# Kernel tuning notes

Measured on AMD Instinct MI355X. Metric: run time of the kernel, lower is better.

The kernel has to match this reference:

```python
import jax, jax.numpy as jnp
import numpy as np

BT = 64  # chunk size (BLOCK_SIZE_C)
EPS = 1e-06


def setup_inputs() -> dict:
    key = jax.random.key(0)
    k1, k2, k3, k4 = jax.random.split(key, 4)
    B, H, S, D = 4, 8, 4096, 128
    q = jax.random.normal(k1, (B, H, S, D), dtype=jnp.float32)
    k = jax.random.normal(k2, (B, H, S, D), dtype=jnp.float32)
    v = jax.random.normal(k3, (B, H, S, D), dtype=jnp.float32)
    beta = jax.random.uniform(k4, (B, H, S), dtype=jnp.float32)
    return {"q": q, "k": k, "v": v, "beta": beta}


def _chunk_gated_delta_fwd(q, k, v, beta):
    # Recurrence: S_t = beta_t * S_{t-1} + k_t (x) v_t ;  o_t = q_t @ S_t
    B, H, S, D = q.shape
    NC = S // BT
    f32 = jnp.float32
    qf = q.astype(f32).reshape(B, H, NC, BT, D)
    kf = k.astype(f32).reshape(B, H, NC, BT, D)
    vf = v.astype(f32).reshape(B, H, NC, BT, D)
    log_beta = jnp.log(beta.astype(f32).reshape(B, H, NC, BT) + EPS)
    cum = jnp.cumsum(log_beta, axis=-1)                     # [B,H,NC,BT]
    tot = cum[..., -1]                                      # [B,H,NC]
    decay_from_start = jnp.exp(cum)                         # [B,H,NC,BT]
    decay_to_end = jnp.exp(tot[..., None] - cum)            # [B,H,NC,BT]
    causal = jnp.tril(jnp.ones((BT, BT), dtype=bool))
    decay_matrix = jnp.exp(cum[..., :, None] - cum[..., None, :])  # [B,H,NC,BT,BT]
    decay_masked = jnp.where(causal, decay_matrix, 0.0)
    # intra-chunk contribution (fully parallel across chunks)
    qk = jnp.einsum('bhcid,bhcjd->bhcij', qf, kf)
    out_intra = jnp.einsum('bhcij,bhcjd->bhcid', qk * decay_masked, vf)
    # per-chunk state-update term: (k * decay_to_end)^T @ v
    upd = jnp.einsum('bhcid,bhcie->bhcde', kf * decay_to_end[..., None], vf)
    # sequential inter-chunk recurrence over chunks
    def step(state, xs):
        qc, dfs_c, tot_c, upd_c = xs
        out_inter = jnp.einsum('bhid,bhde->bhie', qc * dfs_c[..., None], state)
        new_state = state * jnp.exp(tot_c)[..., None, None] + upd_c
        return new_state, out_inter
    xs = (jnp.moveaxis(qf, 2, 0), jnp.moveaxis(decay_from_start, 2, 0),
          jnp.moveaxis(tot, 2, 0), jnp.moveaxis(upd, 2, 0))
    state0 = jnp.zeros((B, H, D, D), dtype=f32)
    _, out_inter = jax.lax.scan(step, state0, xs)           # [NC,B,H,BT,D]
    out = out_intra + jnp.moveaxis(out_inter, 0, 2)
    return out.reshape(B, H, S, D).astype(q.dtype)


def reference(q, k, v, beta):
    return _chunk_gated_delta_fwd(q, k, v, beta)
```

## Files before the change

### kernel.cpp

```cpp
#include <hip/hip_runtime.h>
#include <hip/hip_bf16.h>
#include <math.h>

#define Gp  32
#define Sp  4096
#define Dp  128
#define BTp 64
#define NCp 64

typedef __attribute__((ext_vector_type(8))) short bf16x8;
typedef __attribute__((ext_vector_type(4))) float f32x4;

#define MFMA(a,b,c) __builtin_amdgcn_mfma_f32_16x16x32_bf16((a),(b),(c),0,0,0)

#define TSWZ(d, slot) ((((slot) ^ (((d) & 15) >> 1)) << 3))

__device__ inline unsigned pack2(float lo, float hi) {
    __hip_bfloat162 h = __float22bfloat162_rn(make_float2(lo, hi));
    union { __hip_bfloat162 v; unsigned u; } t; t.v = h; return t.u;
}
__device__ inline float bflo(unsigned u) { union { unsigned u; float f; } t; t.u = u << 16; return t.f; }
__device__ inline float bfhi(unsigned u) { union { unsigned u; float f; } t; t.u = u & 0xffff0000u; return t.f; }

__global__ __launch_bounds__(256) void gdn_beta(
    const float* __restrict__ beta, float* __restrict__ cum_buf,
    float* __restrict__ dte_buf, float* __restrict__ dfs_buf,
    float* __restrict__ tot_buf)
{
    const int tid = threadIdx.x, lane = tid & 63, w = tid >> 6;
    const int cc = blockIdx.x * 4 + w;
    const int g = cc >> 6, c = cc & 63;
    const size_t bbase = (size_t)g * Sp + (size_t)c * BTp;
    float x = logf(beta[bbase + lane] + 1e-6f);
    #pragma unroll
    for (int off = 1; off < 64; off <<= 1) {
        float n = __shfl_up(x, off, 64);
        if (lane >= off) x += n;
    }
    const float tot = __shfl(x, 63, 64);
    cum_buf[bbase + lane] = x;
    dfs_buf[bbase + lane] = expf(x);
    dte_buf[bbase + lane] = expf(tot - x);
    if (lane == 63) tot_buf[g * NCp + c] = tot;
}

__global__ __launch_bounds__(256, 3) void gdn_intra(
    const float* __restrict__ q, const float* __restrict__ k,
    const float* __restrict__ v, const float* __restrict__ cum_buf,
    const float* __restrict__ dte_buf,
    float* __restrict__ out, unsigned short* __restrict__ outi,
    unsigned short* __restrict__ upd)
{
    __shared__ unsigned short s_k [64 * 128];
    __shared__ unsigned short s_vt[128 * 64];
    __shared__ unsigned short s_kt[128 * 64];

    const int blk = blockIdx.x, g = blk >> 6, c = blk & 63;
    const int tid = threadIdx.x, lane = tid & 63, w = tid >> 6;
    const int m16 = lane & 15, quad = lane >> 4;
    const size_t base  = ((size_t)g * Sp + (size_t)c * BTp) * Dp;
    const size_t bbase = (size_t)g * Sp + (size_t)c * BTp;

    const float x = cum_buf[bbase + lane];

    const int dd = 4 * (tid & 31);
    const int rg = tid >> 5;
    const int i0 = 8 * rg;
    const float* kp = k + base + (size_t)i0 * Dp + dd;
    const float* vp = v + base + (size_t)i0 * Dp + dd;
    float4 kx[8], vx[8];
    #pragma unroll
    for (int r = 0; r < 8; ++r) kx[r] = *(const float4*)(kp + (size_t)r * Dp);
    #pragma unroll
    for (int r = 0; r < 8; ++r) vx[r] = *(const float4*)(vp + (size_t)r * Dp);
    const float4 dt0 = *(const float4*)(dte_buf + bbase + i0);
    const float4 dt1 = *(const float4*)(dte_buf + bbase + i0 + 4);

    const float* qrow = q + base + (size_t)(16 * w + m16) * Dp + quad * 8;
    float4 qa[4], qb[4];
    #pragma unroll
    for (int ks = 0; ks < 4; ++ks) {
        qa[ks] = *(const float4*)(qrow + ks * 32);
        qb[ks] = *(const float4*)(qrow + ks * 32 + 4);
    }

    #pragma unroll
    for (int r = 0; r < 8; ++r) {
        const int i = i0 + r;
        const int ad = i * 128 + (((dd >> 3) ^ (i & 15)) << 3) + (dd & 7);
        uint2 pw; pw.x = pack2(kx[r].x, kx[r].y); pw.y = pack2(kx[r].z, kx[r].w);
        *(uint2*)&s_k[ad] = pw;
    }

    {
        uint4 t;
        t.x = pack2(vx[0].x, vx[1].x); t.y = pack2(vx[2].x, vx[3].x);
        t.z = pack2(vx[4].x, vx[5].x); t.w = pack2(vx[6].x, vx[7].x);
        *(uint4*)&s_vt[(dd + 0) * 64 + TSWZ(dd + 0, rg)] = t;
        t.x = pack2(vx[0].y, vx[1].y); t.y = pack2(vx[2].y, vx[3].y);
        t.z = pack2(vx[4].y, vx[5].y); t.w = pack2(vx[6].y, vx[7].y);
        *(uint4*)&s_vt[(dd + 1) * 64 + TSWZ(dd + 1, rg)] = t;
        t.x = pack2(vx[0].z, vx[1].z); t.y = pack2(vx[2].z, vx[3].z);
        t.z = pack2(vx[4].z, vx[5].z); t.w = pack2(vx[6].z, vx[7].z);
        *(uint4*)&s_vt[(dd + 2) * 64 + TSWZ(dd + 2, rg)] = t;
        t.x = pack2(vx[0].w, vx[1].w); t.y = pack2(vx[2].w, vx[3].w);
        t.z = pack2(vx[4].w, vx[5].w); t.w = pack2(vx[6].w, vx[7].w);
        *(uint4*)&s_vt[(dd + 3) * 64 + TSWZ(dd + 3, rg)] = t;
    }

    {
        const float d0 = dt0.x, d1 = dt0.y, d2 = dt0.z, d3 = dt0.w;
        const float d4 = dt1.x, d5 = dt1.y, d6 = dt1.z, d7 = dt1.w;
        uint4 t;
        t.x = pack2(kx[0].x * d0, kx[1].x * d1); t.y = pack2(kx[2].x * d2, kx[3].x * d3);
        t.z = pack2(kx[4].x * d4, kx[5].x * d5); t.w = pack2(kx[6].x * d6, kx[7].x * d7);
        *(uint4*)&s_kt[(dd + 0) * 64 + TSWZ(dd + 0, rg)] = t;
        t.x = pack2(kx[0].y * d0, kx[1].y * d1); t.y = pack2(kx[2].y * d2, kx[3].y * d3);
        t.z = pack2(kx[4].y * d4, kx[5].y * d5); t.w = pack2(kx[6].y * d6, kx[7].y * d7);
        *(uint4*)&s_kt[(dd + 1) * 64 + TSWZ(dd + 1, rg)] = t;
        t.x = pack2(kx[0].z * d0, kx[1].z * d1); t.y = pack2(kx[2].z * d2, kx[3].z * d3);
        t.z = pack2(kx[4].z * d4, kx[5].z * d5); t.w = pack2(kx[6].z * d6, kx[7].z * d7);
        *(uint4*)&s_kt[(dd + 2) * 64 + TSWZ(dd + 2, rg)] = t;
        t.x = pack2(kx[0].w * d0, kx[1].w * d1); t.y = pack2(kx[2].w * d2, kx[3].w * d3);
        t.z = pack2(kx[4].w * d4, kx[5].w * d5); t.w = pack2(kx[6].w * d6, kx[7].w * d7);
        *(uint4*)&s_kt[(dd + 3) * 64 + TSWZ(dd + 3, rg)] = t;
    }

    bf16x8 qf[4];
    #pragma unroll
    for (int ks = 0; ks < 4; ++ks) {
        union { bf16x8 v; unsigned ui[4]; } t;
        t.ui[0] = pack2(qa[ks].x, qa[ks].y); t.ui[1] = pack2(qa[ks].z, qa[ks].w);
        t.ui[2] = pack2(qb[ks].x, qb[ks].y); t.ui[3] = pack2(qb[ks].z, qb[ks].w);
        qf[ks] = t.v;
    }

    __syncthreads();

    f32x4 accP[4] = {};
    #pragma unroll
    for (int nt = 0; nt < 4; ++nt) {
        if (nt <= w) {
            #pragma unroll
            for (int ks = 0; ks < 4; ++ks) {
                const bf16x8 kf = *(const bf16x8*)&s_k[(16 * nt + m16) * 128 + (((quad + 4 * ks) ^ m16) << 3)];
                accP[nt] = MFMA(kf, qf[ks], accP[nt]);
            }
        }
    }

    const float ci = __shfl(x, 16 * w + m16, 64);
    unsigned p_pk[4][2];
    #pragma unroll
    for (int nt = 0; nt < 4; ++nt) { p_pk[nt][0] = 0u; p_pk[nt][1] = 0u; }
    #pragma unroll
    for (int nt = 0; nt < 4; ++nt) {
        if (nt <= w) {
            float pm[4];
            #pragma unroll
            for (int r = 0; r < 4; ++r) {
                const int j = 16 * nt + 4 * quad + r;
                const float cj = __shfl(x, j, 64);
                float val = accP[nt][r] * expf(ci - cj);
                if (nt == w) val = (16 * w + m16 >= j) ? val : 0.f;
                pm[r] = val;
            }
            p_pk[nt][0] = pack2(pm[0], pm[1]);
            p_pk[nt][1] = pack2(pm[2], pm[3]);
        }
    }

    bf16x8 af[2];
    #pragma unroll
    for (int ks = 0; ks < 2; ++ks) {
        if (ks <= (w >> 1)) {
            union { bf16x8 v; unsigned ui[4]; } t;
            #pragma unroll
            for (int m = 0; m < 4; ++m) {
                const int src = m16 + 16 * (2 * (quad & 1) + (m >> 1));
                const unsigned aA = (unsigned)__shfl((int)p_pk[2 * ks][m & 1], src, 64);
                const unsigned aB = (unsigned)__shfl((int)p_pk[2 * ks + 1][m & 1], src, 64);
                t.ui[m] = (quad >> 1) ? aB : aA;
            }
            af[ks] = t.v;
        }
    }

    {
        f32x4 accU[2][8] = {};
        #pragma unroll
        for (int ks = 0; ks < 2; ++ks) {
            const int sw = TSWZ(m16, quad + 4 * ks);
            const bf16x8 b0 = *(const bf16x8*)&s_vt[(16 * (2 * w)     + m16) * 64 + sw];
            const bf16x8 b1 = *(const bf16x8*)&s_vt[(16 * (2 * w + 1) + m16) * 64 + sw];
            #pragma unroll
            for (int nt = 0; nt < 8; ++nt) {
                const bf16x8 a = *(const bf16x8*)&s_kt[(16 * nt + m16) * 64 + sw];
                accU[0][nt] = MFMA(a, b0, accU[0][nt]);
                accU[1][nt] = MFMA(a, b1, accU[1][nt]);
            }
        }
        unsigned short* ub = upd + (size_t)blk * Dp * Dp;
        #pragma unroll
        for (int mt = 0; mt < 2; ++mt) {
            const int e = 16 * (2 * w + mt) + m16;
            #pragma unroll
            for (int nt = 0; nt < 8; ++nt) {
                uint2 pw;
                pw.x = pack2(accU[mt][nt][0], accU[mt][nt][1]);
                pw.y = pack2(accU[mt][nt][2], accU[mt][nt][3]);
                *(uint2*)&ub[(size_t)e * Dp + 16 * nt + 4 * quad] = pw;
            }
        }
    }

    {
        f32x4 accO[8] = {};
        #pragma unroll
        for (int ks = 0; ks < 2; ++ks) {
            if (ks <= (w >> 1)) {
                const int sw = TSWZ(m16, quad + 4 * ks);
                #pragma unroll
                for (int nt = 0; nt < 8; ++nt) {
                    const bf16x8 a = *(const bf16x8*)&s_vt[(16 * nt + m16) * 64 + sw];
                    accO[nt] = MFMA(a, af[ks], accO[nt]);
                }
            }
        }
        const int i = 16 * w + m16;
        if (outi) {
            #pragma unroll
            for (int nt = 0; nt < 8; ++nt) {
                uint2 pw;
                pw.x = pack2(accO[nt][0], accO[nt][1]);
                pw.y = pack2(accO[nt][2], accO[nt][3]);
                *(uint2*)&outi[base + (size_t)i * Dp + 16 * nt + 4 * quad] = pw;
            }
        } else {
            #pragma unroll
            for (int nt = 0; nt < 8; ++nt) {
                float4 st;
                st.x = accO[nt][0]; st.y = accO[nt][1];
                st.z = accO[nt][2]; st.w = accO[nt][3];
                *(float4*)&out[base + (size_t)i * Dp + 16 * nt + 4 * quad] = st;
            }
        }
    }
}

__global__ __launch_bounds__(128) void gdn_scan(
    unsigned short* __restrict__ upd, const float* __restrict__ tot_buf)
{
    const int g = blockIdx.x >> 4, slab = blockIdx.x & 15, tid = threadIdx.x;
    __shared__ float s_e[NCp];
    if (tid < NCp) s_e[tid] = expf(tot_buf[g * NCp + tid]);
    __syncthreads();
    uint4* b = (uint4*)(upd + (size_t)g * NCp * Dp * Dp) + slab * 128 + tid;
    float s0 = 0.f, s1 = 0.f, s2 = 0.f, s3 = 0.f;
    float s4 = 0.f, s5 = 0.f, s6 = 0.f, s7 = 0.f;
    uint4 pf[4];
    #pragma unroll
    for (int j = 0; j < 4; ++j) pf[j] = b[(size_t)j * 2048];
    #pragma unroll
    for (int cc = 0; cc < NCp; ++cc) {
        const uint4 cur = pf[cc & 3];
        if (cc + 4 < NCp) pf[cc & 3] = b[(size_t)(cc + 4) * 2048];
        const float e = s_e[cc];
        uint4 stq;
        stq.x = pack2(s0, s1); stq.y = pack2(s2, s3);
        stq.z = pack2(s4, s5); stq.w = pack2(s6, s7);
        b[(size_t)cc * 2048] = stq;
        s0 = s0 * e + bflo(cur.x); s1 = s1 * e + bfhi(cur.x);
        s2 = s2 * e + bflo(cur.y); s3 = s3 * e + bfhi(cur.y);
        s4 = s4 * e + bflo(cur.z); s5 = s5 * e + bfhi(cur.z);
        s6 = s6 * e + bflo(cur.w); s7 = s7 * e + bfhi(cur.w);
    }
}

__global__ __launch_bounds__(256) void gdn_inter(
    const float* __restrict__ q, const unsigned short* __restrict__ state,
    const float* __restrict__ dfs_buf, const unsigned short* __restrict__ outi,
    float* __restrict__ out)
{
    const int blk = blockIdx.x, g = blk >> 6, c = blk & 63;
    const int tid = threadIdx.x, lane = tid & 63, w = tid >> 6;
    const int m16 = lane & 15, quad = lane >> 4;
    const size_t base  = ((size_t)g * Sp + (size_t)c * BTp) * Dp;
    const size_t bbase = (size_t)g * Sp + (size_t)c * BTp;
    const unsigned short* sb = state + (size_t)blk * Dp * Dp;
    const int i = 16 * w + m16;

    const float scale = dfs_buf[bbase + i];
    bf16x8 qf[4];
    const float* qrow = q + base + (size_t)i * Dp + quad * 8;
    #pragma unroll
    for (int ks = 0; ks < 4; ++ks) {
        const float4 a = *(const float4*)(qrow + ks * 32);
        const float4 b = *(const float4*)(qrow + ks * 32 + 4);
        union { bf16x8 v; unsigned ui[4]; } t;
        t.ui[0] = pack2(a.x * scale, a.y * scale);
        t.ui[1] = pack2(a.z * scale, a.w * scale);
        t.ui[2] = pack2(b.x * scale, b.y * scale);
        t.ui[3] = pack2(b.z * scale, b.w * scale);
        qf[ks] = t.v;
    }

    float ovf[8][4];
    if (outi) {
        #pragma unroll
        for (int nt = 0; nt < 8; ++nt) {
            const uint2 pw = *(const uint2*)&outi[base + (size_t)i * Dp + 16 * nt + 4 * quad];
            ovf[nt][0] = bflo(pw.x); ovf[nt][1] = bfhi(pw.x);
            ovf[nt][2] = bflo(pw.y); ovf[nt][3] = bfhi(pw.y);
        }
    } else {
        #pragma unroll
        for (int nt = 0; nt < 8; ++nt) {
            const float4 o = *(const float4*)&out[base + (size_t)i * Dp + 16 * nt + 4 * quad];
            ovf[nt][0] = o.x; ovf[nt][1] = o.y; ovf[nt][2] = o.z; ovf[nt][3] = o.w;
        }
    }

    f32x4 acc[8] = {};
    #pragma unroll
    for (int ks = 0; ks < 4; ++ks) {
        bf16x8 afr[8];
        #pragma unroll
        for (int nt = 0; nt < 8; ++nt)
            afr[nt] = *(const bf16x8*)(sb + (16 * nt + m16) * Dp + quad * 8 + ks * 32);
        #pragma unroll
        for (int nt = 0; nt < 8; ++nt)
            acc[nt] = MFMA(afr[nt], qf[ks], acc[nt]);
    }
    #pragma unroll
    for (int nt = 0; nt < 8; ++nt) {
        float4 st;
        st.x = ovf[nt][0] + acc[nt][0]; st.y = ovf[nt][1] + acc[nt][1];
        st.z = ovf[nt][2] + acc[nt][2]; st.w = ovf[nt][3] + acc[nt][3];
        *(float4*)&out[base + (size_t)i * Dp + 16 * nt + 4 * quad] = st;
    }
}

extern "C" void kernel_launch(void* const* d_in, const int* in_sizes, int n_in,
                              void* d_out, int out_size, void* d_ws, size_t ws_size,
                              hipStream_t stream) {
    const float* q    = (const float*)d_in[0];
    const float* k    = (const float*)d_in[1];
    const float* v    = (const float*)d_in[2];
    const float* beta = (const float*)d_in[3];
    float* out = (float*)d_out;

    unsigned short* upd = (unsigned short*)d_ws;
    float* tot_buf = (float*)(upd + (size_t)Gp * NCp * Dp * Dp);
    float* dfs_buf = tot_buf + Gp * NCp;
    float* cum_buf = dfs_buf + (size_t)Gp * Sp;
    float* dte_buf = cum_buf + (size_t)Gp * Sp;
    unsigned short* outi = (unsigned short*)(dte_buf + (size_t)Gp * Sp);
    const size_t need = (size_t)((char*)(outi + (size_t)Gp * Sp * Dp) - (char*)d_ws);
    if (ws_size < need) outi = nullptr;

    gdn_beta <<<Gp * NCp / 4, 256, 0, stream>>>(beta, cum_buf, dte_buf, dfs_buf, tot_buf);
    gdn_intra<<<Gp * NCp, 256, 0, stream>>>(q, k, v, cum_buf, dte_buf, out, outi, upd);
    gdn_scan <<<Gp * 16, 128, 0, stream>>>(upd, tot_buf);
    gdn_inter<<<Gp * NCp, 256, 0, stream>>>(q, upd, dfs_buf, outi, out);
}
```

Baseline: 302.1 us.

## Process two chunks per intra block with prefetch and cache scaled bf16 q

The intra kernel now handles two consecutive chunks per block. It loads the second chunk's k/v/q into registers while the first chunk is being computed, so global-load latency can overlap with MFMA work. The intra kernel also writes a decay-scaled bf16 copy of q to the workspace, so the inter kernel reads half the bytes and skips the rescale. The costs are more register pressure (launch bounds drop from 3 to 2 blocks per CU), half as many blocks, extra workspace writes, and rounding q to bf16 twice.

Result: slower. 310.0 us (+2.6%).

```diff
diff --git a/kernel.cpp b/kernel.cpp
--- a/kernel.cpp
+++ b/kernel.cpp
@@ -44,46 +44,13 @@
     if (lane == 63) tot_buf[g * NCp + c] = tot;
 }
 
-__global__ __launch_bounds__(256, 3) void gdn_intra(
-    const float* __restrict__ q, const float* __restrict__ k,
-    const float* __restrict__ v, const float* __restrict__ cum_buf,
-    const float* __restrict__ dte_buf,
-    float* __restrict__ out, unsigned short* __restrict__ outi,
-    unsigned short* __restrict__ upd)
-{
-    __shared__ unsigned short s_k [64 * 128];
-    __shared__ unsigned short s_vt[128 * 64];
-    __shared__ unsigned short s_kt[128 * 64];
-
-    const int blk = blockIdx.x, g = blk >> 6, c = blk & 63;
-    const int tid = threadIdx.x, lane = tid & 63, w = tid >> 6;
-    const int m16 = lane & 15, quad = lane >> 4;
-    const size_t base  = ((size_t)g * Sp + (size_t)c * BTp) * Dp;
-    const size_t bbase = (size_t)g * Sp + (size_t)c * BTp;
-
-    const float x = cum_buf[bbase + lane];
-
-    const int dd = 4 * (tid & 31);
-    const int rg = tid >> 5;
+__device__ __forceinline__ void stage_chunk(
+    unsigned short* __restrict__ s_k, unsigned short* __restrict__ s_vt,
+    unsigned short* __restrict__ s_kt,
+    int dd, int rg, const float4* kx, const float4* vx,
+    const float4 dt0, const float4 dt1)
+{
     const int i0 = 8 * rg;
-    const float* kp = k + base + (size_t)i0 * Dp + dd;
-    const float* vp = v + base + (size_t)i0 * Dp + dd;
-    float4 kx[8], vx[8];
-    #pragma unroll
-    for (int r = 0; r < 8; ++r) kx[r] = *(const float4*)(kp + (size_t)r * Dp);
-    #pragma unroll
-    for (int r = 0; r < 8; ++r) vx[r] = *(const float4*)(vp + (size_t)r * Dp);
-    const float4 dt0 = *(const float4*)(dte_buf + bbase + i0);
-    const float4 dt1 = *(const float4*)(dte_buf + bbase + i0 + 4);
-
-    const float* qrow = q + base + (size_t)(16 * w + m16) * Dp + quad * 8;
-    float4 qa[4], qb[4];
-    #pragma unroll
-    for (int ks = 0; ks < 4; ++ks) {
-        qa[ks] = *(const float4*)(qrow + ks * 32);
-        qb[ks] = *(const float4*)(qrow + ks * 32 + 4);
-    }
-
     #pragma unroll
     for (int r = 0; r < 8; ++r) {
         const int i = i0 + r;
@@ -91,7 +58,6 @@
         uint2 pw; pw.x = pack2(kx[r].x, kx[r].y); pw.y = pack2(kx[r].z, kx[r].w);
         *(uint2*)&s_k[ad] = pw;
     }
-
     {
         uint4 t;
         t.x = pack2(vx[0].x, vx[1].x); t.y = pack2(vx[2].x, vx[3].x);
@@ -107,7 +73,6 @@
         t.z = pack2(vx[4].w, vx[5].w); t.w = pack2(vx[6].w, vx[7].w);
         *(uint4*)&s_vt[(dd + 3) * 64 + TSWZ(dd + 3, rg)] = t;
     }
-
     {
         const float d0 = dt0.x, d1 = dt0.y, d2 = dt0.z, d3 = dt0.w;
         const float d4 = dt1.x, d5 = dt1.y, d6 = dt1.z, d7 = dt1.w;
@@ -125,8 +90,10 @@
         t.z = pack2(kx[4].w * d4, kx[5].w * d5); t.w = pack2(kx[6].w * d6, kx[7].w * d7);
         *(uint4*)&s_kt[(dd + 3) * 64 + TSWZ(dd + 3, rg)] = t;
     }
-
-    bf16x8 qf[4];
+}
+
+__device__ __forceinline__ void pack_q(const float4* qa, const float4* qb, bf16x8* qf)
+{
     #pragma unroll
     for (int ks = 0; ks < 4; ++ks) {
         union { bf16x8 v; unsigned ui[4]; } t;
@@ -134,9 +101,17 @@
         t.ui[2] = pack2(qb[ks].x, qb[ks].y); t.ui[3] = pack2(qb[ks].z, qb[ks].w);
         qf[ks] = t.v;
     }
-
-    __syncthreads();
-
+}
+
+__device__ __forceinline__ void intra_compute(
+    const float x, const bf16x8* qf,
+    const unsigned short* s_k, const unsigned short* s_vt,
+    const unsigned short* s_kt,
+    const int w, const int m16, const int quad,
+    const size_t base, const size_t cid,
+    float* __restrict__ out, unsigned short* __restrict__ outi,
+    unsigned short* __restrict__ upd, unsigned short* __restrict__ qs)
+{
     f32x4 accP[4] = {};
     #pragma unroll
     for (int nt = 0; nt < 4; ++nt) {
@@ -170,6 +145,20 @@
         }
     }
 
+    if (qs) {
+        const float sc = expf(ci);
+        #pragma unroll
+        for (int ks = 0; ks < 4; ++ks) {
+            union { bf16x8 v; unsigned ui[4]; } t; t.v = qf[ks];
+            uint4 o;
+            o.x = pack2(bflo(t.ui[0]) * sc, bfhi(t.ui[0]) * sc);
+            o.y = pack2(bflo(t.ui[1]) * sc, bfhi(t.ui[1]) * sc);
+            o.z = pack2(bflo(t.ui[2]) * sc, bfhi(t.ui[2]) * sc);
+            o.w = pack2(bflo(t.ui[3]) * sc, bfhi(t.ui[3]) * sc);
+            *(uint4*)&qs[base + (size_t)(16 * w + m16) * Dp + quad * 8 + ks * 32] = o;
+        }
+    }
+
     bf16x8 af[2];
     #pragma unroll
     for (int ks = 0; ks < 2; ++ks) {
@@ -200,7 +189,7 @@
                 accU[1][nt] = MFMA(a, b1, accU[1][nt]);
             }
         }
-        unsigned short* ub = upd + (size_t)blk * Dp * Dp;
+        unsigned short* ub = upd + cid * (size_t)(Dp * Dp);
         #pragma unroll
         for (int mt = 0; mt < 2; ++mt) {
             const int e = 16 * (2 * w + mt) + m16;
@@ -246,6 +235,93 @@
             }
         }
     }
+}
+
+__global__ __launch_bounds__(256, 2) void gdn_intra(
+    const float* __restrict__ q, const float* __restrict__ k,
+    const float* __restrict__ v, const float* __restrict__ cum_buf,
+    const float* __restrict__ dte_buf,
+    float* __restrict__ out, unsigned short* __restrict__ outi,
+    unsigned short* __restrict__ upd, unsigned short* __restrict__ qs)
+{
+    __shared__ unsigned short s_k [64 * 128];
+    __shared__ unsigned short s_vt[128 * 64];
+    __shared__ unsigned short s_kt[128 * 64];
+
+    const int blk = blockIdx.x, g = blk >> 5, pr = blk & 31;
+    const int c0 = 2 * pr;
+    const int tid = threadIdx.x, lane = tid & 63, w = tid >> 6;
+    const int m16 = lane & 15, quad = lane >> 4;
+    const int dd = 4 * (tid & 31), rg = tid >> 5, i0 = 8 * rg;
+
+    const size_t cid0  = (size_t)g * NCp + c0, cid1 = cid0 + 1;
+    const size_t bb0   = (size_t)g * Sp + (size_t)c0 * BTp, bb1 = bb0 + BTp;
+    const size_t base0 = bb0 * Dp, base1 = bb1 * Dp;
+
+    const float x0 = cum_buf[bb0 + lane];
+    float4 kx[8], vx[8];
+    {
+        const float* kp = k + base0 + (size_t)i0 * Dp + dd;
+        const float* vp = v + base0 + (size_t)i0 * Dp + dd;
+        #pragma unroll
+        for (int r = 0; r < 8; ++r) kx[r] = *(const float4*)(kp + (size_t)r * Dp);
+        #pragma unroll
+        for (int r = 0; r < 8; ++r) vx[r] = *(const float4*)(vp + (size_t)r * Dp);
+    }
+    const float4 dt00 = *(const float4*)(dte_buf + bb0 + i0);
+    const float4 dt01 = *(const float4*)(dte_buf + bb0 + i0 + 4);
+    float4 qa[4], qb[4];
+    {
+        const float* qrow = q + base0 + (size_t)(16 * w + m16) * Dp + quad * 8;
+        #pragma unroll
+        for (int ks = 0; ks < 4; ++ks) {
+            qa[ks] = *(const float4*)(qrow + ks * 32);
+            qb[ks] = *(const float4*)(qrow + ks * 32 + 4);
+        }
+    }
+
+    stage_chunk(s_k, s_vt, s_kt, dd, rg, kx, vx, dt00, dt01);
+    bf16x8 qf0[4];
+    pack_q(qa, qb, qf0);
+
+    const float x1 = cum_buf[bb1 + lane];
+    float4 kx1[8], vx1[8];
+    {
+        const float* kp = k + base1 + (size_t)i0 * Dp + dd;
+        const float* vp = v + base1 + (size_t)i0 * Dp + dd;
+        #pragma unroll
+        for (int r = 0; r < 8; ++r) kx1[r] = *(const float4*)(kp + (size_t)r * Dp);
+        #pragma unroll
+        for (int r = 0; r < 8; ++r) vx1[r] = *(const float4*)(vp + (size_t)r * Dp);
+    }
+    const float4 dt10 = *(const float4*)(dte_buf + bb1 + i0);
+    const float4 dt11 = *(const float4*)(dte_buf + bb1 + i0 + 4);
+
+    __syncthreads();
+
+    float4 qa1[4], qb1[4];
+    {
+        const float* qrow = q + base1 + (size_t)(16 * w + m16) * Dp + quad * 8;
+        #pragma unroll
+        for (int ks = 0; ks < 4; ++ks) {
+            qa1[ks] = *(const float4*)(qrow + ks * 32);
+            qb1[ks] = *(const float4*)(qrow + ks * 32 + 4);
+        }
+    }
+
+    intra_compute(x0, qf0, s_k, s_vt, s_kt, w, m16, quad,
+                  base0, cid0, out, outi, upd, qs);
+
+    __syncthreads();
+
+    stage_chunk(s_k, s_vt, s_kt, dd, rg, kx1, vx1, dt10, dt11);
+    bf16x8 qf1[4];
+    pack_q(qa1, qb1, qf1);
+
+    __syncthreads();
+
+    intra_compute(x1, qf1, s_k, s_vt, s_kt, w, m16, quad,
+                  base1, cid1, out, outi, upd, qs);
 }
 
 __global__ __launch_bounds__(128) void gdn_scan(
@@ -280,7 +356,7 @@
 __global__ __launch_bounds__(256) void gdn_inter(
     const float* __restrict__ q, const unsigned short* __restrict__ state,
     const float* __restrict__ dfs_buf, const unsigned short* __restrict__ outi,
-    float* __restrict__ out)
+    const unsigned short* __restrict__ qs, float* __restrict__ out)
 {
     const int blk = blockIdx.x, g = blk >> 6, c = blk & 63;
     const int tid = threadIdx.x, lane = tid & 63, w = tid >> 6;
@@ -290,19 +366,26 @@
     const unsigned short* sb = state + (size_t)blk * Dp * Dp;
     const int i = 16 * w + m16;
 
-    const float scale = dfs_buf[bbase + i];
     bf16x8 qf[4];
-    const float* qrow = q + base + (size_t)i * Dp + quad * 8;
-    #pragma unroll
-    for (int ks = 0; ks < 4; ++ks) {
-        const float4 a = *(const float4*)(qrow + ks * 32);
-        const float4 b = *(const float4*)(qrow + ks * 32 + 4);
-        union { bf16x8 v; unsigned ui[4]; } t;
-        t.ui[0] = pack2(a.x * scale, a.y * scale);
-        t.ui[1] = pack2(a.z * scale, a.w * scale);
-        t.ui[2] = pack2(b.x * scale, b.y * scale);
-        t.ui[3] = pack2(b.z * scale, b.w * scale);
-        qf[ks] = t.v;
+    if (qs) {
+        const unsigned short* qrow = qs + base + (size_t)i * Dp + quad * 8;
+        #pragma unroll
+        for (int ks = 0; ks < 4; ++ks)
+            qf[ks] = *(const bf16x8*)(qrow + ks * 32);
+    } else {
+        const float scale = dfs_buf[bbase + i];
+        const float* qrow = q + base + (size_t)i * Dp + quad * 8;
+        #pragma unroll
+        for (int ks = 0; ks < 4; ++ks) {
+            const float4 a = *(const float4*)(qrow + ks * 32);
+            const float4 b = *(const float4*)(qrow + ks * 32 + 4);
+            union { bf16x8 v; unsigned ui[4]; } t;
+            t.ui[0] = pack2(a.x * scale, a.y * scale);
+            t.ui[1] = pack2(a.z * scale, a.w * scale);
+            t.ui[2] = pack2(b.x * scale, b.y * scale);
+            t.ui[3] = pack2(b.z * scale, b.w * scale);
+            qf[ks] = t.v;
+        }
     }
 
     float ovf[8][4];
@@ -356,11 +439,14 @@
     float* cum_buf = dfs_buf + (size_t)Gp * Sp;
     float* dte_buf = cum_buf + (size_t)Gp * Sp;
     unsigned short* outi = (unsigned short*)(dte_buf + (size_t)Gp * Sp);
-    const size_t need = (size_t)((char*)(outi + (size_t)Gp * Sp * Dp) - (char*)d_ws);
-    if (ws_size < need) outi = nullptr;
+    unsigned short* qs   = outi + (size_t)Gp * Sp * Dp;
+    const size_t need_oi = (size_t)((char*)(outi + (size_t)Gp * Sp * Dp) - (char*)d_ws);
+    const size_t need_qs = (size_t)((char*)(qs   + (size_t)Gp * Sp * Dp) - (char*)d_ws);
+    if (ws_size < need_oi) outi = nullptr;
+    if (ws_size < need_qs) qs   = nullptr;
 
     gdn_beta <<<Gp * NCp / 4, 256, 0, stream>>>(beta, cum_buf, dte_buf, dfs_buf, tot_buf);
-    gdn_intra<<<Gp * NCp, 256, 0, stream>>>(q, k, v, cum_buf, dte_buf, out, outi, upd);
+    gdn_intra<<<Gp * NCp / 2, 256, 0, stream>>>(q, k, v, cum_buf, dte_buf, out, outi, upd, qs);
     gdn_scan <<<Gp * 16, 128, 0, stream>>>(upd, tot_buf);
-    gdn_inter<<<Gp * NCp, 256, 0, stream>>>(q, upd, dfs_buf, outi, out);
-}
+    gdn_inter<<<Gp * NCp, 256, 0, stream>>>(q, upd, dfs_buf, outi, qs, out);
+}
```

## Fuse inter-chunk scan and inter output into one sequential per-head kernel

Applied to the files above, without the earlier changes.

The intra kernel now also writes a decay-scaled bf16 copy of q. A new gdn_fused kernel replaces the separate scan and inter kernels. Each block owns one head and a 32-column slice of the state, keeps that state in fp32 registers, and walks all 64 chunks in order. At each chunk it computes q·S with MFMA, adds the intra output and updates the state, with the next chunk's loads double-buffered. This removes the materialised per-chunk state round trip and one launch. The cost is only 128 blocks doing a serial 64-step loop, which may underfill the GPU, plus an extra q workspace buffer.

New measurement: 349.2 us. 1.16x slower.

```diff
diff --git a/kernel.cpp b/kernel.cpp
--- a/kernel.cpp
+++ b/kernel.cpp
@@ -44,46 +44,13 @@
     if (lane == 63) tot_buf[g * NCp + c] = tot;
 }
 
-__global__ __launch_bounds__(256, 3) void gdn_intra(
-    const float* __restrict__ q, const float* __restrict__ k,
-    const float* __restrict__ v, const float* __restrict__ cum_buf,
-    const float* __restrict__ dte_buf,
-    float* __restrict__ out, unsigned short* __restrict__ outi,
-    unsigned short* __restrict__ upd)
-{
-    __shared__ unsigned short s_k [64 * 128];
-    __shared__ unsigned short s_vt[128 * 64];
-    __shared__ unsigned short s_kt[128 * 64];
-
-    const int blk = blockIdx.x, g = blk >> 6, c = blk & 63;
-    const int tid = threadIdx.x, lane = tid & 63, w = tid >> 6;
-    const int m16 = lane & 15, quad = lane >> 4;
-    const size_t base  = ((size_t)g * Sp + (size_t)c * BTp) * Dp;
-    const size_t bbase = (size_t)g * Sp + (size_t)c * BTp;
-
-    const float x = cum_buf[bbase + lane];
-
-    const int dd = 4 * (tid & 31);
-    const int rg = tid >> 5;
+__device__ __forceinline__ void stage_chunk(
+    unsigned short* __restrict__ s_k, unsigned short* __restrict__ s_vt,
+    unsigned short* __restrict__ s_kt,
+    int dd, int rg, const float4* kx, const float4* vx,
+    const float4 dt0, const float4 dt1)
+{
     const int i0 = 8 * rg;
-    const float* kp = k + base + (size_t)i0 * Dp + dd;
-    const float* vp = v + base + (size_t)i0 * Dp + dd;
-    float4 kx[8], vx[8];
-    #pragma unroll
-    for (int r = 0; r < 8; ++r) kx[r] = *(const float4*)(kp + (size_t)r * Dp);
-    #pragma unroll
-    for (int r = 0; r < 8; ++r) vx[r] = *(const float4*)(vp + (size_t)r * Dp);
-    const float4 dt0 = *(const float4*)(dte_buf + bbase + i0);
-    const float4 dt1 = *(const float4*)(dte_buf + bbase + i0 + 4);
-
-    const float* qrow = q + base + (size_t)(16 * w + m16) * Dp + quad * 8;
-    float4 qa[4], qb[4];
-    #pragma unroll
-    for (int ks = 0; ks < 4; ++ks) {
-        qa[ks] = *(const float4*)(qrow + ks * 32);
-        qb[ks] = *(const float4*)(qrow + ks * 32 + 4);
-    }
-
     #pragma unroll
     for (int r = 0; r < 8; ++r) {
         const int i = i0 + r;
@@ -91,7 +58,6 @@
         uint2 pw; pw.x = pack2(kx[r].x, kx[r].y); pw.y = pack2(kx[r].z, kx[r].w);
         *(uint2*)&s_k[ad] = pw;
     }
-
     {
         uint4 t;
         t.x = pack2(vx[0].x, vx[1].x); t.y = pack2(vx[2].x, vx[3].x);
@@ -107,7 +73,6 @@
         t.z = pack2(vx[4].w, vx[5].w); t.w = pack2(vx[6].w, vx[7].w);
         *(uint4*)&s_vt[(dd + 3) * 64 + TSWZ(dd + 3, rg)] = t;
     }
-
     {
         const float d0 = dt0.x, d1 = dt0.y, d2 = dt0.z, d3 = dt0.w;
         const float d4 = dt1.x, d5 = dt1.y, d6 = dt1.z, d7 = dt1.w;
@@ -125,8 +90,10 @@
         t.z = pack2(kx[4].w * d4, kx[5].w * d5); t.w = pack2(kx[6].w * d6, kx[7].w * d7);
         *(uint4*)&s_kt[(dd + 3) * 64 + TSWZ(dd + 3, rg)] = t;
     }
-
-    bf16x8 qf[4];
+}
+
+__device__ __forceinline__ void pack_q(const float4* qa, const float4* qb, bf16x8* qf)
+{
     #pragma unroll
     for (int ks = 0; ks < 4; ++ks) {
         union { bf16x8 v; unsigned ui[4]; } t;
@@ -134,9 +101,17 @@
         t.ui[2] = pack2(qb[ks].x, qb[ks].y); t.ui[3] = pack2(qb[ks].z, qb[ks].w);
         qf[ks] = t.v;
     }
-
-    __syncthreads();
-
+}
+
+__device__ __forceinline__ void intra_compute(
+    const float x, const bf16x8* qf,
+    const unsigned short* s_k, const unsigned short* s_vt,
+    const unsigned short* s_kt,
+    const int w, const int m16, const int quad,
+    const size_t base, const size_t cid,
+    float* __restrict__ out, unsigned short* __restrict__ outi,
+    unsigned short* __restrict__ upd, unsigned short* __restrict__ qs)
+{
     f32x4 accP[4] = {};
     #pragma unroll
     for (int nt = 0; nt < 4; ++nt) {
@@ -170,6 +145,20 @@
         }
     }
 
+    if (qs) {
+        const float sc = expf(ci);
+        #pragma unroll
+        for (int ks = 0; ks < 4; ++ks) {
+            union { bf16x8 v; unsigned ui[4]; } t; t.v = qf[ks];
+            uint4 o;
+            o.x = pack2(bflo(t.ui[0]) * sc, bfhi(t.ui[0]) * sc);
+            o.y = pack2(bflo(t.ui[1]) * sc, bfhi(t.ui[1]) * sc);
+            o.z = pack2(bflo(t.ui[2]) * sc, bfhi(t.ui[2]) * sc);
+            o.w = pack2(bflo(t.ui[3]) * sc, bfhi(t.ui[3]) * sc);
+            *(uint4*)&qs[base + (size_t)(16 * w + m16) * Dp + quad * 8 + ks * 32] = o;
+        }
+    }
+
     bf16x8 af[2];
     #pragma unroll
     for (int ks = 0; ks < 2; ++ks) {
@@ -200,7 +189,7 @@
                 accU[1][nt] = MFMA(a, b1, accU[1][nt]);
             }
         }
-        unsigned short* ub = upd + (size_t)blk * Dp * Dp;
+        unsigned short* ub = upd + cid * (size_t)(Dp * Dp);
         #pragma unroll
         for (int mt = 0; mt < 2; ++mt) {
             const int e = 16 * (2 * w + mt) + m16;
@@ -245,6 +234,149 @@
                 *(float4*)&out[base + (size_t)i * Dp + 16 * nt + 4 * quad] = st;
             }
         }
+    }
+}
+
+__global__ __launch_bounds__(256, 3) void gdn_intra(
+    const float* __restrict__ q, const float* __restrict__ k,
+    const float* __restrict__ v, const float* __restrict__ cum_buf,
+    const float* __restrict__ dte_buf,
+    float* __restrict__ out, unsigned short* __restrict__ outi,
+    unsigned short* __restrict__ upd, unsigned short* __restrict__ qs)
+{
+    __shared__ unsigned short s_k [64 * 128];
+    __shared__ unsigned short s_vt[128 * 64];
+    __shared__ unsigned short s_kt[128 * 64];
+
+    const int blk = blockIdx.x, g = blk >> 6, c = blk & 63;
+    const int tid = threadIdx.x, lane = tid & 63, w = tid >> 6;
+    const int m16 = lane & 15, quad = lane >> 4;
+    const int dd = 4 * (tid & 31), rg = tid >> 5, i0 = 8 * rg;
+    const size_t bbase = (size_t)g * Sp + (size_t)c * BTp;
+    const size_t base  = bbase * Dp;
+    const size_t cid   = (size_t)g * NCp + c;
+
+    const float x = cum_buf[bbase + lane];
+    float4 kx[8], vx[8];
+    {
+        const float* kp = k + base + (size_t)i0 * Dp + dd;
+        const float* vp = v + base + (size_t)i0 * Dp + dd;
+        #pragma unroll
+        for (int r = 0; r < 8; ++r) kx[r] = *(const float4*)(kp + (size_t)r * Dp);
+        #pragma unroll
+        for (int r = 0; r < 8; ++r) vx[r] = *(const float4*)(vp + (size_t)r * Dp);
+    }
+    const float4 dt0 = *(const float4*)(dte_buf + bbase + i0);
+    const float4 dt1 = *(const float4*)(dte_buf + bbase + i0 + 4);
+    float4 qa[4], qb[4];
+    {
+        const float* qrow = q + base + (size_t)(16 * w + m16) * Dp + quad * 8;
+        #pragma unroll
+        for (int ks = 0; ks < 4; ++ks) {
+            qa[ks] = *(const float4*)(qrow + ks * 32);
+            qb[ks] = *(const float4*)(qrow + ks * 32 + 4);
+        }
+    }
+
+    stage_chunk(s_k, s_vt, s_kt, dd, rg, kx, vx, dt0, dt1);
+    bf16x8 qf[4];
+    pack_q(qa, qb, qf);
+
+    __syncthreads();
+
+    intra_compute(x, qf, s_k, s_vt, s_kt, w, m16, quad,
+                  base, cid, out, outi, upd, qs);
+}
+
+#define UPDK(Sfp, Sbp, Uv) do {                                              \
+    Sfp[0] = Sfp[0]*ec + bflo(Uv.x); Sfp[1] = Sfp[1]*ec + bfhi(Uv.x);        \
+    Sfp[2] = Sfp[2]*ec + bflo(Uv.y); Sfp[3] = Sfp[3]*ec + bfhi(Uv.y);        \
+    Sfp[4] = Sfp[4]*ec + bflo(Uv.z); Sfp[5] = Sfp[5]*ec + bfhi(Uv.z);        \
+    Sfp[6] = Sfp[6]*ec + bflo(Uv.w); Sfp[7] = Sfp[7]*ec + bfhi(Uv.w);        \
+    union { bf16x8 v; unsigned ui[4]; } tpk;                                  \
+    tpk.ui[0] = pack2(Sfp[0], Sfp[1]); tpk.ui[1] = pack2(Sfp[2], Sfp[3]);    \
+    tpk.ui[2] = pack2(Sfp[4], Sfp[5]); tpk.ui[3] = pack2(Sfp[6], Sfp[7]);    \
+    Sbp = tpk.v;                                                              \
+} while (0)
+
+#define LOADCH(c, U, QA, OI) do {                                            \
+    const size_t co_ = (size_t)(c) * (BTp * Dp);                             \
+    const size_t cu_ = (size_t)(c) * (Dp * Dp);                              \
+    _Pragma("unroll")                                                        \
+    for (int ks = 0; ks < 4; ++ks) {                                         \
+        U[0][ks] = *(const uint4*)(up0 + cu_ + ks * 32);                     \
+        U[1][ks] = *(const uint4*)(up1 + cu_ + ks * 32);                     \
+        QA[ks]   = *(const bf16x8*)(qp + co_ + ks * 32);                     \
+    }                                                                        \
+    OI[0] = *(const uint2*)(op + co_ + E0 + 4 * quad);                       \
+    OI[1] = *(const uint2*)(op + co_ + E0 + 16 + 4 * quad);                  \
+} while (0)
+
+#define STEPCH(c, U, QA, OI) do {                                            \
+    f32x4 a0 = {}, a1 = {};                                                  \
+    _Pragma("unroll")                                                        \
+    for (int ks = 0; ks < 4; ++ks) {                                         \
+        a0 = MFMA(Sb0[ks], QA[ks], a0);                                      \
+        a1 = MFMA(Sb1[ks], QA[ks], a1);                                      \
+    }                                                                        \
+    const size_t co_ = (size_t)(c) * (BTp * Dp);                             \
+    float4 s0, s1;                                                           \
+    s0.x = bflo(OI[0].x) + a0[0]; s0.y = bfhi(OI[0].x) + a0[1];              \
+    s0.z = bflo(OI[0].y) + a0[2]; s0.w = bfhi(OI[0].y) + a0[3];              \
+    s1.x = bflo(OI[1].x) + a1[0]; s1.y = bfhi(OI[1].x) + a1[1];              \
+    s1.z = bflo(OI[1].y) + a1[2]; s1.w = bfhi(OI[1].y) + a1[3];              \
+    *(float4*)(wp + co_ + E0 + 4 * quad) = s0;                               \
+    *(float4*)(wp + co_ + E0 + 16 + 4 * quad) = s1;                          \
+    const float ec = s_e[c];                                                 \
+    _Pragma("unroll")                                                        \
+    for (int ks = 0; ks < 4; ++ks) {                                         \
+        UPDK((&Sf0[ks * 8]), Sb0[ks], U[0][ks]);                             \
+        UPDK((&Sf1[ks * 8]), Sb1[ks], U[1][ks]);                             \
+    }                                                                        \
+} while (0)
+
+__global__ __launch_bounds__(256) void gdn_fused(
+    const unsigned short* __restrict__ upd, const unsigned short* __restrict__ qs,
+    const unsigned short* __restrict__ outi, const float* __restrict__ tot_buf,
+    float* __restrict__ out)
+{
+    const int g = blockIdx.x >> 2, eb = blockIdx.x & 3;
+    const int E0 = eb * 32;
+    const int tid = threadIdx.x, lane = tid & 63, w = tid >> 6;
+    const int m16 = lane & 15, quad = lane >> 4;
+
+    __shared__ float s_e[NCp];
+    if (tid < NCp) s_e[tid] = expf(tot_buf[g * NCp + tid]);
+    __syncthreads();
+
+    const size_t gq = (size_t)g * Sp * Dp;
+    const int i = 16 * w + m16;
+    const unsigned short* qp  = qs   + gq + (size_t)i * Dp + quad * 8;
+    const unsigned short* op  = outi + gq + (size_t)i * Dp;
+    float*                wp  = out  + gq + (size_t)i * Dp;
+    const unsigned short* up0 = upd + (size_t)g * NCp * Dp * Dp
+                                    + (size_t)(E0 + m16) * Dp + quad * 8;
+    const unsigned short* up1 = up0 + 16 * Dp;
+
+    float Sf0[32], Sf1[32];
+    #pragma unroll
+    for (int j = 0; j < 32; ++j) { Sf0[j] = 0.f; Sf1[j] = 0.f; }
+    bf16x8 Sb0[4], Sb1[4];
+    #pragma unroll
+    for (int ks = 0; ks < 4; ++ks) {
+        bf16x8 z = {0, 0, 0, 0, 0, 0, 0, 0};
+        Sb0[ks] = z; Sb1[ks] = z;
+    }
+
+    uint4 Ua[2][4]; bf16x8 Qa[4]; uint2 Oa[2];
+    uint4 Ub[2][4]; bf16x8 Qb[4]; uint2 Ob[2];
+    LOADCH(0, Ua, Qa, Oa);
+    #pragma unroll 1
+    for (int c = 0; c < NCp; c += 2) {
+        LOADCH(c + 1, Ub, Qb, Ob);
+        STEPCH(c, Ua, Qa, Oa);
+        if (c + 2 < NCp) LOADCH(c + 2, Ua, Qa, Oa);
+        STEPCH(c + 1, Ub, Qb, Ob);
     }
 }
 
@@ -279,8 +411,7 @@
 
 __global__ __launch_bounds__(256) void gdn_inter(
     const float* __restrict__ q, const unsigned short* __restrict__ state,
-    const float* __restrict__ dfs_buf, const unsigned short* __restrict__ outi,
-    float* __restrict__ out)
+    const float* __restrict__ dfs_buf, float* __restrict__ out)
 {
     const int blk = blockIdx.x, g = blk >> 6, c = blk & 63;
     const int tid = threadIdx.x, lane = tid & 63, w = tid >> 6;
@@ -304,23 +435,10 @@
         t.ui[3] = pack2(b.z * scale, b.w * scale);
         qf[ks] = t.v;
     }
-
-    float ovf[8][4];
-    if (outi) {
-        #pragma unroll
-        for (int nt = 0; nt < 8; ++nt) {
-            const uint2 pw = *(const uint2*)&outi[base + (size_t)i * Dp + 16 * nt + 4 * quad];
-            ovf[nt][0] = bflo(pw.x); ovf[nt][1] = bfhi(pw.x);
-            ovf[nt][2] = bflo(pw.y); ovf[nt][3] = bfhi(pw.y);
-        }
-    } else {
-        #pragma unroll
-        for (int nt = 0; nt < 8; ++nt) {
-            const float4 o = *(const float4*)&out[base + (size_t)i * Dp + 16 * nt + 4 * quad];
-            ovf[nt][0] = o.x; ovf[nt][1] = o.y; ovf[nt][2] = o.z; ovf[nt][3] = o.w;
-        }
-    }
-
+    float4 ov[8];
+    #pragma unroll
+    for (int nt = 0; nt < 8; ++nt)
+        ov[nt] = *(const float4*)&out[base + (size_t)i * Dp + 16 * nt + 4 * quad];
     f32x4 acc[8] = {};
     #pragma unroll
     for (int ks = 0; ks < 4; ++ks) {
@@ -335,8 +453,8 @@
     #pragma unroll
     for (int nt = 0; nt < 8; ++nt) {
         float4 st;
-        st.x = ovf[nt][0] + acc[nt][0]; st.y = ovf[nt][1] + acc[nt][1];
-        st.z = ovf[nt][2] + acc[nt][2]; st.w = ovf[nt][3] + acc[nt][3];
+        st.x = ov[nt].x + acc[nt][0]; st.y = ov[nt].y + acc[nt][1];
+        st.z = ov[nt].z + acc[nt][2]; st.w = ov[nt].w + acc[nt][3];
         *(float4*)&out[base + (size_t)i * Dp + 16 * nt + 4 * quad] = st;
     }
 }
@@ -356,11 +474,19 @@
     float* cum_buf = dfs_buf + (size_t)Gp * Sp;
     float* dte_buf = cum_buf + (size_t)Gp * Sp;
     unsigned short* outi = (unsigned short*)(dte_buf + (size_t)Gp * Sp);
-    const size_t need = (size_t)((char*)(outi + (size_t)Gp * Sp * Dp) - (char*)d_ws);
-    if (ws_size < need) outi = nullptr;
+    unsigned short* qs   = outi + (size_t)Gp * Sp * Dp;
+    const size_t need = (size_t)((char*)(qs + (size_t)Gp * Sp * Dp) - (char*)d_ws);
+    const bool fused_ok = (ws_size >= need);
 
     gdn_beta <<<Gp * NCp / 4, 256, 0, stream>>>(beta, cum_buf, dte_buf, dfs_buf, tot_buf);
-    gdn_intra<<<Gp * NCp, 256, 0, stream>>>(q, k, v, cum_buf, dte_buf, out, outi, upd);
-    gdn_scan <<<Gp * 16, 128, 0, stream>>>(upd, tot_buf);
-    gdn_inter<<<Gp * NCp, 256, 0, stream>>>(q, upd, dfs_buf, outi, out);
-}
+    if (fused_ok) {
+        gdn_intra<<<Gp * NCp, 256, 0, stream>>>(q, k, v, cum_buf, dte_buf,
+                                                out, outi, upd, qs);
+        gdn_fused<<<Gp * 4, 256, 0, stream>>>(upd, qs, outi, tot_buf, out);
+    } else {
+        gdn_intra<<<Gp * NCp, 256, 0, stream>>>(q, k, v, cum_buf, dte_buf,
+                                                out, nullptr, upd, nullptr);
+        gdn_scan <<<Gp * 16, 128, 0, stream>>>(upd, tot_buf);
+        gdn_inter<<<Gp * NCp, 256, 0, stream>>>(q, upd, dfs_buf, out);
+    }
+}
```
